# Performance work log

Hardware: AMD Instinct MI355X
Metric: run time of the kernel (lower is better)

Reference implementation:

```python
import jax, jax.numpy as jnp
import numpy as np

ALPHA = 0.5  # leak/integration rate of the EI cell

B, L, D = 512, 64, 784
N_EXC, N_INH, N_CLS = 128, 32, 10


def setup_inputs() -> dict:
    key = jax.random.key(0)
    ks = jax.random.split(key, 11)
    s_in = 1.0 / np.sqrt(D)
    s_e = 1.0 / np.sqrt(N_EXC)
    s_i = 1.0 / np.sqrt(N_INH)
    return {
        "x_seq": jax.random.normal(ks[0], (B, L, D), jnp.float32),
        "Wxe": jax.random.normal(ks[1], (N_EXC, D), jnp.float32) * s_in,
        "Wxi": jax.random.normal(ks[2], (N_INH, D), jnp.float32) * s_in,
        "Wee": jax.random.normal(ks[3], (N_EXC, N_EXC), jnp.float32) * s_e,
        "Wie": jax.random.normal(ks[4], (N_EXC, N_INH), jnp.float32) * s_i,
        "Wei": jax.random.normal(ks[5], (N_INH, N_EXC), jnp.float32) * s_e,
        "Wii": jax.random.normal(ks[6], (N_INH, N_INH), jnp.float32) * s_i,
        "be": jax.random.normal(ks[7], (N_EXC,), jnp.float32) * 0.01,
        "bi": jax.random.normal(ks[8], (N_INH,), jnp.float32) * 0.01,
        "W_ro": jax.random.normal(ks[9], (N_CLS, N_EXC), jnp.float32) * s_e,
        "b_ro": jax.random.normal(ks[10], (N_CLS,), jnp.float32) * 0.01,
    }


def reference(x_seq, Wxe, Wxi, Wee, Wie, Wei, Wii, be, bi, W_ro, b_ro):
    # Dale's law: rectify weight magnitudes so exc/inh signs are structural.
    Wxe_p, Wxi_p = jax.nn.relu(Wxe), jax.nn.relu(Wxi)
    Wee_p, Wie_p = jax.nn.relu(Wee), jax.nn.relu(Wie)
    Wei_p, Wii_p = jax.nn.relu(Wei), jax.nn.relu(Wii)

    def step(carry, x_t):  # x_t: [B, D]
        e, i = carry
        r_e = jax.nn.relu(e)
        r_i = jax.nn.relu(i)
        exc_e = x_t @ Wxe_p.T + r_e @ Wee_p.T          # [B, n_exc]
        inh_e = r_i @ Wie_p.T                           # [B, n_exc]
        exc_i = x_t @ Wxi_p.T + r_e @ Wei_p.T           # [B, n_inh]
        inh_i = r_i @ Wii_p.T                           # [B, n_inh]
        e_new = (1.0 - ALPHA) * e + ALPHA * (exc_e - inh_e + be)
        i_new = (1.0 - ALPHA) * i + ALPHA * (exc_i - inh_i + bi)
        r_e_new = jax.nn.relu(e_new)
        r_i_new = jax.nn.relu(i_new)
        bal_e = exc_e - inh_e
        bal_i = exc_i - inh_i
        logits_t = r_e_new @ W_ro.T + b_ro              # readout(F.relu(e))
        return (e_new, i_new), (logits_t, r_e_new, r_i_new, bal_e, bal_i)

    Bn = x_seq.shape[0]
    e0 = jnp.zeros((Bn, Wee.shape[0]), x_seq.dtype)
    i0 = jnp.zeros((Bn, Wii.shape[0]), x_seq.dtype)
    _, outs = jax.lax.scan(step, (e0, i0), jnp.swapaxes(x_seq, 0, 1))  # time-major
    logits_seq, r_e_seq, r_i_seq, bal_e_seq, bal_i_seq = (
        jnp.swapaxes(o, 0, 1) for o in outs)  # back to [B, L, ...]
    return logits_seq, logits_seq[:, -1, :], r_e_seq, r_i_seq, bal_e_seq, bal_i_seq
```

## Files before the change

### kernel.cpp

```cpp
#include <hip/hip_runtime.h>

#define NE 128
#define NI 32
#define NT 160
#define NC 10
#define BB 512
#define LL 64
#define DD 784
#define KP 800
#define MM (BB*LL)

#define G_OFF   0
#define G_SZ    (NT*NT)
#define WH_OFF  (G_OFF + G_SZ)
#define WL_OFF  (WH_OFF + 64000)
#define U_OFF   (WL_OFF + 64000)
#define U_SZ    (MM*NT)

#define O_LOGITS 0
#define O_LAST   327680
#define O_RE     332800
#define O_RI     4527104
#define O_BALE   5575680
#define O_BALI   9769984

#define LDS_BARRIER() asm volatile("s_waitcnt lgkmcnt(0)\n\ts_barrier" ::: "memory")

typedef __attribute__((ext_vector_type(8))) short short8;
typedef __attribute__((ext_vector_type(4))) float af4;

static __device__ __forceinline__ unsigned short f2bf(float f) {
  unsigned u = __float_as_uint(f);
  return (unsigned short)((u + 0x7FFFu + ((u >> 16) & 1u)) >> 16);
}
static __device__ __forceinline__ float bf2f(unsigned short h) {
  return __uint_as_float((unsigned)h << 16);
}

static __device__ __forceinline__ void cvt_split8(const float* f, short8& ah, short8& al) {
  union { short8 s; unsigned u[4]; } H, L;
  #pragma unroll
  for (int p = 0; p < 4; ++p) {
    float lo = f[2*p], hi = f[2*p+1];
    unsigned h;
    asm("v_cvt_pk_bf16_f32 %0, %1, %2" : "=v"(h) : "v"(lo), "v"(hi));
    float rl = lo - __uint_as_float(h << 16);
    float rh = hi - __uint_as_float(h & 0xffff0000u);
    unsigned l;
    asm("v_cvt_pk_bf16_f32 %0, %1, %2" : "=v"(l) : "v"(rl), "v"(rh));
    H.u[p] = h; L.u[p] = l;
  }
  ah = H.s; al = L.s;
}

__global__ void prep_kernel(const float* __restrict__ Wxe, const float* __restrict__ Wxi,
                            const float* __restrict__ Wee, const float* __restrict__ Wie,
                            const float* __restrict__ Wei, const float* __restrict__ Wii,
                            float* __restrict__ ws) {
  int idx = blockIdx.x * blockDim.x + threadIdx.x;
  const int total = G_SZ + NT * KP;
  if (idx >= total) return;
  if (idx < G_SZ) {
    int k = idx / NT, j = idx % NT;
    float g;
    if (j < NE) {
      if (k < NE) g =  fmaxf(Wee[j*NE + k], 0.f);
      else        g = -fmaxf(Wie[j*NI + (k-NE)], 0.f);
    } else {
      int ji = j - NE;
      if (k < NE) g =  fmaxf(Wei[ji*NE + k], 0.f);
      else        g = -fmaxf(Wii[ji*NI + (k-NE)], 0.f);
    }
    ws[G_OFF + k*NT + j] = g;
  } else {
    int t = idx - G_SZ;
    int n = t / KP, k = t - n * KP;
    float v = 0.f;
    if (k < DD)
      v = (n < NE) ? fmaxf(Wxe[n*DD + k], 0.f) : fmaxf(Wxi[(n-NE)*DD + k], 0.f);
    unsigned short h = f2bf(v);
    unsigned short l = f2bf(v - bf2f(h));
    ((unsigned short*)(ws + WH_OFF))[t] = h;
    ((unsigned short*)(ws + WL_OFF))[t] = l;
  }
}

__global__ __launch_bounds__(256, 2) void gemm_kernel(const float* __restrict__ X,
                                                      const float* __restrict__ ws,
                                                      float* __restrict__ U) {
  const int tid  = threadIdx.x;
  const int lane = tid & 63;
  const int wave = tid >> 6;
  const int n16  = lane & 15;
  const int quad = lane >> 4;
  const int mbase = blockIdx.x * 64 + wave * 16;

  const unsigned short* Wh = (const unsigned short*)(ws + WH_OFF);
  const unsigned short* Wl = (const unsigned short*)(ws + WL_OFF);

  af4 acc[10];
  #pragma unroll
  for (int nt = 0; nt < 10; ++nt)
    #pragma unroll
    for (int r = 0; r < 4; ++r) acc[nt][r] = 0.f;

  const float* xrow = X + (size_t)(mbase + n16) * DD;

  float fa[8];
  {
    const int kb = quad * 8;
    float4 v0 = *(const float4*)(xrow + kb);
    float4 v1 = *(const float4*)(xrow + kb + 4);
    fa[0]=v0.x; fa[1]=v0.y; fa[2]=v0.z; fa[3]=v0.w;
    fa[4]=v1.x; fa[5]=v1.y; fa[6]=v1.z; fa[7]=v1.w;
  }

  for (int ks = 0; ks < 24; ++ks) {
    const int kb = ks * 32 + quad * 8;
    float nf[8] = {0,0,0,0,0,0,0,0};
    {
      const int nkb = kb + 32;
      if (nkb < DD) {
        float4 v0 = *(const float4*)(xrow + nkb);
        float4 v1 = *(const float4*)(xrow + nkb + 4);
        nf[0]=v0.x; nf[1]=v0.y; nf[2]=v0.z; nf[3]=v0.w;
        nf[4]=v1.x; nf[5]=v1.y; nf[6]=v1.z; nf[7]=v1.w;
      }
    }
    short8 bh[10], bl[10];
    #pragma unroll
    for (int nt = 0; nt < 10; ++nt) {
      const size_t off = (size_t)(nt * 16 + n16) * KP + kb;
      bh[nt] = *(const short8*)(Wh + off);
      bl[nt] = *(const short8*)(Wl + off);
    }
    short8 ah, al;
    cvt_split8(fa, ah, al);
    #pragma unroll
    for (int nt = 0; nt < 10; ++nt) {
      acc[nt] = __builtin_amdgcn_mfma_f32_16x16x32_bf16(ah, bh[nt], acc[nt], 0, 0, 0);
      acc[nt] = __builtin_amdgcn_mfma_f32_16x16x32_bf16(ah, bl[nt], acc[nt], 0, 0, 0);
      acc[nt] = __builtin_amdgcn_mfma_f32_16x16x32_bf16(al, bh[nt], acc[nt], 0, 0, 0);
    }
    #pragma unroll
    for (int j = 0; j < 8; ++j) fa[j] = nf[j];
  }

  {
    const int kb = 768 + quad * 8;
    short8 bh[10], bl[10];
    #pragma unroll
    for (int nt = 0; nt < 10; ++nt) {
      const size_t off = (size_t)(nt * 16 + n16) * KP + kb;
      bh[nt] = *(const short8*)(Wh + off);
      bl[nt] = *(const short8*)(Wl + off);
    }
    short8 ah, al;
    cvt_split8(fa, ah, al);
    #pragma unroll
    for (int nt = 0; nt < 10; ++nt) {
      acc[nt] = __builtin_amdgcn_mfma_f32_16x16x32_bf16(ah, bh[nt], acc[nt], 0, 0, 0);
      acc[nt] = __builtin_amdgcn_mfma_f32_16x16x32_bf16(ah, bl[nt], acc[nt], 0, 0, 0);
      acc[nt] = __builtin_amdgcn_mfma_f32_16x16x32_bf16(al, bh[nt], acc[nt], 0, 0, 0);
    }
  }

  #pragma unroll
  for (int nt = 0; nt < 10; ++nt)
    #pragma unroll
    for (int r = 0; r < 4; ++r) {
      const int row = mbase + quad * 4 + r;
      U[(size_t)row * NT + nt * 16 + n16] = acc[nt][r];
    }
}

__global__ __launch_bounds__(256, 2) void recur_kernel(
    const float* __restrict__ ws,
    const float* __restrict__ be, const float* __restrict__ bi,
    float* __restrict__ out) {
  __shared__ float rbuf[2][NT];
  __shared__ float balbuf[2][NT];
  __shared__ float biasL[NT];

  const int tid  = threadIdx.x;
  const int lane = tid & 63;
  const int wave = tid >> 6;
  const int jc   = (wave << 3) | (lane & 7);
  const int kc   = (lane >> 3) & 7;
  const int j0   = jc * 5;
  const int k0   = kc * 20;
  const int b    = blockIdx.x;

  const float* G = ws + G_OFF;
  const float* U = ws + U_OFF;

  float g[20][5];
  #pragma unroll
  for (int kk = 0; kk < 20; ++kk)
    #pragma unroll
    for (int c = 0; c < 5; ++c)
      g[kk][c] = G[(size_t)(k0 + kk) * NT + j0 + c];

  if (tid < NT) biasL[tid] = (tid < NE) ? be[tid] : bi[tid - NE];
  for (int i = tid; i < 2 * NT; i += 256) (&rbuf[0][0])[i] = 0.f;

  const bool owner = (kc == 0);
  float u[5];
  if (owner) {
    const size_t ub = ((size_t)b * LL) * NT + j0;
    #pragma unroll
    for (int c = 0; c < 5; ++c) u[c] = U[ub + c];
  }
  float s[5];
  #pragma unroll
  for (int c = 0; c < 5; ++c) s[c] = 0.f;

  __syncthreads();

  for (int l = 0; l < LL; ++l) {
    const int p = l & 1;
    if (l > 0) {
      const size_t ob = (size_t)b * LL + (l - 1);
      if (tid < NE) {
        out[O_RE   + ob * NE + tid] = rbuf[p][tid];
        out[O_BALE + ob * NE + tid] = balbuf[p][tid];
      } else if (tid < NT) {
        const int j2 = tid - NE;
        out[O_RI   + ob * NI + j2] = rbuf[p][NE + j2];
        out[O_BALI + ob * NI + j2] = balbuf[p][NE + j2];
      }
    }
    float nu[5];
    if (owner && l + 1 < LL) {
      const size_t nb = ((size_t)b * LL + (l + 1)) * NT + j0;
      #pragma unroll
      for (int c = 0; c < 5; ++c) nu[c] = U[nb + c];
    }
    float a[5];
    #pragma unroll
    for (int c = 0; c < 5; ++c) a[c] = 0.f;
    #pragma unroll
    for (int kk4 = 0; kk4 < 5; ++kk4) {
      float4 rv = *(const float4*)(&rbuf[p][k0 + kk4 * 4]);
      #pragma unroll
      for (int c = 0; c < 5; ++c)
        a[c] += rv.x * g[kk4*4+0][c] + rv.y * g[kk4*4+1][c]
              + rv.z * g[kk4*4+2][c] + rv.w * g[kk4*4+3][c];
    }
    #pragma unroll
    for (int c = 0; c < 5; ++c) {
      float v = a[c];
      v += __shfl_xor(v, 8, 64);
      v += __shfl_xor(v, 16, 64);
      v += __shfl_xor(v, 32, 64);
      a[c] = v;
    }
    if (owner) {
      #pragma unroll
      for (int c = 0; c < 5; ++c) {
        float bal = a[c] + u[c];
        balbuf[1 - p][j0 + c] = bal;
        float sn = 0.5f * (s[c] + bal + biasL[j0 + c]);
        s[c] = sn;
        rbuf[1 - p][j0 + c] = fmaxf(sn, 0.f);
      }
      #pragma unroll
      for (int c = 0; c < 5; ++c) u[c] = nu[c];
    }
    LDS_BARRIER();
  }
  {
    const size_t ob = (size_t)b * LL + 63;
    if (tid < NE) {
      out[O_RE   + ob * NE + tid] = rbuf[0][tid];
      out[O_BALE + ob * NE + tid] = balbuf[0][tid];
    } else if (tid < NT) {
      const int j2 = tid - NE;
      out[O_RI   + ob * NI + j2] = rbuf[0][NE + j2];
      out[O_BALI + ob * NI + j2] = balbuf[0][NE + j2];
    }
  }
}

__global__ __launch_bounds__(256) void logits_kernel(const float* __restrict__ Wro,
                                                     const float* __restrict__ bro,
                                                     float* __restrict__ out) {
  __shared__ float WroL[NC * 132];
  __shared__ float broL[NC];
  const int tid = threadIdx.x;
  for (int i = tid; i < NC * NE; i += 256) {
    int c = i >> 7, k = i & 127;
    WroL[c * 132 + k] = Wro[i];
  }
  if (tid < NC) broL[tid] = bro[tid];
  __syncthreads();
  const int idx = blockIdx.x * 256 + tid;
  const int m = idx / 10, c = idx - m * 10;
  const float* re = out + O_RE + (size_t)m * NE;
  float v = broL[c];
  #pragma unroll
  for (int t4 = 0; t4 < 32; ++t4) {
    float4 rv = *(const float4*)(re + t4 * 4);
    float4 wv = *(const float4*)(&WroL[c * 132 + t4 * 4]);
    v += rv.x * wv.x + rv.y * wv.y + rv.z * wv.z + rv.w * wv.w;
  }
  out[O_LOGITS + (size_t)m * NC + c] = v;
  if ((m & 63) == 63) out[O_LAST + (size_t)(m >> 6) * NC + c] = v;
}

extern "C" void kernel_launch(void* const* d_in, const int* in_sizes, int n_in,
                              void* d_out, int out_size, void* d_ws, size_t ws_size,
                              hipStream_t stream) {
  const float* x   = (const float*)d_in[0];
  const float* Wxe = (const float*)d_in[1];
  const float* Wxi = (const float*)d_in[2];
  const float* Wee = (const float*)d_in[3];
  const float* Wie = (const float*)d_in[4];
  const float* Wei = (const float*)d_in[5];
  const float* Wii = (const float*)d_in[6];
  const float* be  = (const float*)d_in[7];
  const float* bi  = (const float*)d_in[8];
  const float* Wro = (const float*)d_in[9];
  const float* bro = (const float*)d_in[10];
  float* ws  = (float*)d_ws;
  float* out = (float*)d_out;

  hipLaunchKernelGGL(prep_kernel, dim3((G_SZ + NT*KP + 255)/256), dim3(256), 0, stream,
                     Wxe, Wxi, Wee, Wie, Wei, Wii, ws);
  hipLaunchKernelGGL(gemm_kernel, dim3(MM/64), dim3(256), 0, stream,
                     x, ws, ws + U_OFF);
  hipLaunchKernelGGL(recur_kernel, dim3(BB), dim3(256), 0, stream,
                     ws, be, bi, out);
  hipLaunchKernelGGL(logits_kernel, dim3(MM * NC / 256), dim3(256), 0, stream,
                     Wro, bro, out);
}
```

Measured before the change: 319.2 us.

## Stage split-bf16 weights in swizzled LDS with double-buffered async loads

The input-projection GEMM now stages each 32-wide K slice of the high/low bf16 weight planes into shared memory using direct global-to-LDS loads, double-buffered and XOR-swizzled to avoid bank conflicts. Each wave also computes two 16-row M subtiles, so one weight fragment feeds twice as many MFMAs, and the block tile grows to 128 rows, halving the grid. This cuts redundant global weight traffic per block. It costs more registers and LDS, lowers the launch-bounds occupancy hint to one block per SM, and adds a barrier per K step.

```diff
diff --git a/kernel.cpp b/kernel.cpp
--- a/kernel.cpp
+++ b/kernel.cpp
@@ -85,93 +85,124 @@
   }
 }
 
-__global__ __launch_bounds__(256, 2) void gemm_kernel(const float* __restrict__ X,
+static __device__ __forceinline__ void stage_tile(const unsigned short* __restrict__ Wh,
+                                                  const unsigned short* __restrict__ Wl,
+                                                  unsigned short* dstBase, int kb, int tid) {
+  #pragma unroll
+  for (int i = 0; i < 5; ++i) {
+    const int idx = i * 256 + tid;
+    const int row = idx >> 3;
+    const int phys = idx & 7;
+    const int logical = phys ^ (row & 7);
+    const unsigned short* src =
+        ((logical & 4) ? Wl : Wh) + (size_t)row * KP + kb + (logical & 3) * 8;
+    __builtin_amdgcn_global_load_lds(
+        (const __attribute__((address_space(1))) unsigned int*)src,
+        (__attribute__((address_space(3))) unsigned int*)(dstBase + idx * 8),
+        16, 0, 0);
+  }
+}
+
+__global__ __launch_bounds__(256, 1) void gemm_kernel(const float* __restrict__ X,
                                                       const float* __restrict__ ws,
                                                       float* __restrict__ U) {
+  __shared__ unsigned short tile[2][10240];
+
   const int tid  = threadIdx.x;
   const int lane = tid & 63;
   const int wave = tid >> 6;
   const int n16  = lane & 15;
   const int quad = lane >> 4;
-  const int mbase = blockIdx.x * 64 + wave * 16;
+  const int sw   = n16 & 7;
+  const int mbase = blockIdx.x * 128 + wave * 32;
 
   const unsigned short* Wh = (const unsigned short*)(ws + WH_OFF);
   const unsigned short* Wl = (const unsigned short*)(ws + WL_OFF);
 
-  af4 acc[10];
-  #pragma unroll
-  for (int nt = 0; nt < 10; ++nt)
-    #pragma unroll
-    for (int r = 0; r < 4; ++r) acc[nt][r] = 0.f;
-
-  const float* xrow = X + (size_t)(mbase + n16) * DD;
-
-  float fa[8];
+  af4 acc[2][10];
+  #pragma unroll
+  for (int ms = 0; ms < 2; ++ms)
+    #pragma unroll
+    for (int nt = 0; nt < 10; ++nt)
+      #pragma unroll
+      for (int r = 0; r < 4; ++r) acc[ms][nt][r] = 0.f;
+
+  const float* xr0 = X + (size_t)(mbase + n16) * DD;
+  const float* xr1 = xr0 + (size_t)16 * DD;
+
+  stage_tile(Wh, Wl, tile[0], 0, tid);
+  float fa0[8], fa1[8];
   {
     const int kb = quad * 8;
-    float4 v0 = *(const float4*)(xrow + kb);
-    float4 v1 = *(const float4*)(xrow + kb + 4);
-    fa[0]=v0.x; fa[1]=v0.y; fa[2]=v0.z; fa[3]=v0.w;
-    fa[4]=v1.x; fa[5]=v1.y; fa[6]=v1.z; fa[7]=v1.w;
-  }
-
-  for (int ks = 0; ks < 24; ++ks) {
-    const int kb = ks * 32 + quad * 8;
-    float nf[8] = {0,0,0,0,0,0,0,0};
+    float4 v0 = *(const float4*)(xr0 + kb);
+    float4 v1 = *(const float4*)(xr0 + kb + 4);
+    fa0[0]=v0.x; fa0[1]=v0.y; fa0[2]=v0.z; fa0[3]=v0.w;
+    fa0[4]=v1.x; fa0[5]=v1.y; fa0[6]=v1.z; fa0[7]=v1.w;
+    float4 w0 = *(const float4*)(xr1 + kb);
+    float4 w1 = *(const float4*)(xr1 + kb + 4);
+    fa1[0]=w0.x; fa1[1]=w0.y; fa1[2]=w0.z; fa1[3]=w0.w;
+    fa1[4]=w1.x; fa1[5]=w1.y; fa1[6]=w1.z; fa1[7]=w1.w;
+  }
+  __syncthreads();
+
+  for (int ks = 0; ks < 25; ++ks) {
+    const int cur = ks & 1;
+    if (ks < 24) stage_tile(Wh, Wl, tile[cur ^ 1], (ks + 1) * 32, tid);
+
+    float nf0[8] = {0,0,0,0,0,0,0,0};
+    float nf1[8] = {0,0,0,0,0,0,0,0};
     {
-      const int nkb = kb + 32;
+      const int nkb = (ks + 1) * 32 + quad * 8;
       if (nkb < DD) {
-        float4 v0 = *(const float4*)(xrow + nkb);
-        float4 v1 = *(const float4*)(xrow + nkb + 4);
-        nf[0]=v0.x; nf[1]=v0.y; nf[2]=v0.z; nf[3]=v0.w;
-        nf[4]=v1.x; nf[5]=v1.y; nf[6]=v1.z; nf[7]=v1.w;
+        float4 v0 = *(const float4*)(xr0 + nkb);
+        float4 v1 = *(const float4*)(xr0 + nkb + 4);
+        nf0[0]=v0.x; nf0[1]=v0.y; nf0[2]=v0.z; nf0[3]=v0.w;
+        nf0[4]=v1.x; nf0[5]=v1.y; nf0[6]=v1.z; nf0[7]=v1.w;
+        float4 w0 = *(const float4*)(xr1 + nkb);
+        float4 w1 = *(const float4*)(xr1 + nkb + 4);
+        nf1[0]=w0.x; nf1[1]=w0.y; nf1[2]=w0.z; nf1[3]=w0.w;
+        nf1[4]=w1.x; nf1[5]=w1.y; nf1[6]=w1.z; nf1[7]=w1.w;
       }
     }
+
     short8 bh[10], bl[10];
+    const unsigned short* tb = tile[cur];
     #pragma unroll
     for (int nt = 0; nt < 10; ++nt) {
-      const size_t off = (size_t)(nt * 16 + n16) * KP + kb;
-      bh[nt] = *(const short8*)(Wh + off);
-      bl[nt] = *(const short8*)(Wl + off);
-    }
-    short8 ah, al;
-    cvt_split8(fa, ah, al);
+      const int ro = (nt * 16 + n16) * 64;
+      bh[nt] = *(const short8*)(tb + ro + ((quad ^ sw) << 3));
+      bl[nt] = *(const short8*)(tb + ro + (((4 | quad) ^ sw) << 3));
+    }
+
+    short8 ah0, al0, ah1, al1;
+    cvt_split8(fa0, ah0, al0);
+    cvt_split8(fa1, ah1, al1);
+
     #pragma unroll
     for (int nt = 0; nt < 10; ++nt) {
-      acc[nt] = __builtin_amdgcn_mfma_f32_16x16x32_bf16(ah, bh[nt], acc[nt], 0, 0, 0);
-      acc[nt] = __builtin_amdgcn_mfma_f32_16x16x32_bf16(ah, bl[nt], acc[nt], 0, 0, 0);
-      acc[nt] = __builtin_amdgcn_mfma_f32_16x16x32_bf16(al, bh[nt], acc[nt], 0, 0, 0);
-    }
-    #pragma unroll
-    for (int j = 0; j < 8; ++j) fa[j] = nf[j];
-  }
-
-  {
-    const int kb = 768 + quad * 8;
-    short8 bh[10], bl[10];
-    #pragma unroll
-    for (int nt = 0; nt < 10; ++nt) {
-      const size_t off = (size_t)(nt * 16 + n16) * KP + kb;
-      bh[nt] = *(const short8*)(Wh + off);
-      bl[nt] = *(const short8*)(Wl + off);
-    }
-    short8 ah, al;
-    cvt_split8(fa, ah, al);
-    #pragma unroll
-    for (int nt = 0; nt < 10; ++nt) {
-      acc[nt] = __builtin_amdgcn_mfma_f32_16x16x32_bf16(ah, bh[nt], acc[nt], 0, 0, 0);
-      acc[nt] = __builtin_amdgcn_mfma_f32_16x16x32_bf16(ah, bl[nt], acc[nt], 0, 0, 0);
-      acc[nt] = __builtin_amdgcn_mfma_f32_16x16x32_bf16(al, bh[nt], acc[nt], 0, 0, 0);
-    }
-  }
-
-  #pragma unroll
-  for (int nt = 0; nt < 10; ++nt)
-    #pragma unroll
-    for (int r = 0; r < 4; ++r) {
-      const int row = mbase + quad * 4 + r;
-      U[(size_t)row * NT + nt * 16 + n16] = acc[nt][r];
-    }
+      acc[0][nt] = __builtin_amdgcn_mfma_f32_16x16x32_bf16(ah0, bh[nt], acc[0][nt], 0, 0, 0);
+      acc[1][nt] = __builtin_amdgcn_mfma_f32_16x16x32_bf16(ah1, bh[nt], acc[1][nt], 0, 0, 0);
+      acc[0][nt] = __builtin_amdgcn_mfma_f32_16x16x32_bf16(ah0, bl[nt], acc[0][nt], 0, 0, 0);
+      acc[1][nt] = __builtin_amdgcn_mfma_f32_16x16x32_bf16(ah1, bl[nt], acc[1][nt], 0, 0, 0);
+      acc[0][nt] = __builtin_amdgcn_mfma_f32_16x16x32_bf16(al0, bh[nt], acc[0][nt], 0, 0, 0);
+      acc[1][nt] = __builtin_amdgcn_mfma_f32_16x16x32_bf16(al1, bh[nt], acc[1][nt], 0, 0, 0);
+    }
+
+    #pragma unroll
+    for (int j = 0; j < 8; ++j) { fa0[j] = nf0[j]; fa1[j] = nf1[j]; }
+
+    __syncthreads();
+  }
+
+  #pragma unroll
+  for (int ms = 0; ms < 2; ++ms)
+    #pragma unroll
+    for (int nt = 0; nt < 10; ++nt)
+      #pragma unroll
+      for (int r = 0; r < 4; ++r) {
+        const int row = mbase + ms * 16 + quad * 4 + r;
+        U[(size_t)row * NT + nt * 16 + n16] = acc[ms][nt][r];
+      }
 }
 
 __global__ __launch_bounds__(256, 2) void recur_kernel(
@@ -327,7 +358,7 @@
 
   hipLaunchKernelGGL(prep_kernel, dim3((G_SZ + NT*KP + 255)/256), dim3(256), 0, stream,
                      Wxe, Wxi, Wee, Wie, Wei, Wii, ws);
-  hipLaunchKernelGGL(gemm_kernel, dim3(MM/64), dim3(256), 0, stream,
+  hipLaunchKernelGGL(gemm_kernel, dim3(MM/128), dim3(256), 0, stream,
                      x, ws, ws + U_OFF);
   hipLaunchKernelGGL(recur_kernel, dim3(BB), dim3(256), 0, stream,
                      ws, be, bi, out);
```

After: 277.4 us. -13.1%, faster.
